# Kernel tuning notes

Hardware: AMD Instinct MI355X
Metric: run time of the kernel (lower is better)

## Reference

```python
import jax, jax.numpy as jnp
import numpy as np

D_MODEL = 2048
NUM_HEADS = 16
THETA = 10000.0


def setup_inputs() -> dict:
    key = jax.random.key(0)
    ks = jax.random.split(key, 5)
    bs, S, d = 4, 2048, D_MODEL
    std = (2.0 / (d + d)) ** 0.5
    x = jax.random.normal(ks[0], (bs, S, d), dtype=jnp.float32)
    wq = jax.random.normal(ks[1], (d, d), dtype=jnp.float32) * std
    wk = jax.random.normal(ks[2], (d, d), dtype=jnp.float32) * std
    wv = jax.random.normal(ks[3], (d, d), dtype=jnp.float32) * std
    wo = jax.random.normal(ks[4], (d, d), dtype=jnp.float32) * std
    return {"x": x, "wq": wq, "wk": wk, "wv": wv, "wo": wo}


def _rope(t, cos, sin):
    # t: (bs, H, S, d_k); cos/sin: (S, d_k) interleaved-duplicated
    # rotate_half: (-x1, x0, -x3, x2, ...)
    x_even = t[..., 0::2]
    x_odd = t[..., 1::2]
    rot = jnp.stack((-x_odd, x_even), axis=-1).reshape(t.shape)
    return t * cos + rot * sin


def reference(x, wq, wk, wv, wo):
    bs, S, d = x.shape
    H = NUM_HEADS
    dk = d // H
    # QKV projections (Linear has no bias; weight stored (out, in), applied as x @ W.T)
    q = (x @ wq.T).reshape(bs, S, H, dk).transpose(0, 2, 1, 3)  # (bs,H,S,dk)
    k = (x @ wk.T).reshape(bs, S, H, dk).transpose(0, 2, 1, 3)
    v = (x @ wv.T).reshape(bs, S, H, dk).transpose(0, 2, 1, 3)

    # RoPE tables (interleaved convention)
    half = dk // 2
    inv_freq = THETA ** (-2.0 * jnp.arange(half, dtype=jnp.float32) / dk)  # (half,)
    pos = jnp.arange(S, dtype=jnp.float32)
    ang = pos[:, None] * inv_freq[None, :]  # (S, half)
    cos = jnp.repeat(jnp.cos(ang), 2, axis=-1)  # (S, dk), (c0,c0,c1,c1,...)
    sin = jnp.repeat(jnp.sin(ang), 2, axis=-1)
    q = _rope(q, cos, sin)
    k = _rope(k, cos, sin)

    scale = 1.0 / jnp.sqrt(jnp.asarray(dk, dtype=x.dtype))
    attn = jnp.einsum("bhqd,bhkd->bhqk", q, k) * scale  # (bs,H,S,S)
    causal = jnp.tril(jnp.ones((S, S), dtype=bool))
    attn = jnp.where(causal, attn, -jnp.inf)
    probs = jax.nn.softmax(attn, axis=-1)
    out = jnp.einsum("bhqk,bhkd->bhqd", probs, v)  # (bs,H,S,dk)
    out = out.transpose(0, 2, 1, 3).reshape(bs, S, d)
    return out @ wo.T
```

## Files before the change

### kernel.cpp

```cpp
#include <hip/hip_runtime.h>
#include <hip/hip_bf16.h>
#include <cstdint>
#include <cstddef>

typedef unsigned short u16;
typedef unsigned int u32;
typedef __attribute__((ext_vector_type(8))) short short8;
typedef __attribute__((ext_vector_type(4))) short bfx4;
typedef __attribute__((ext_vector_type(4))) float f32x4;

#define D_MODEL 2048
#define SEQ     2048
#define BATCH   4
#define NHEADS  16
#define DKH     128
#define NTOK    (BATCH*SEQ)

typedef const __attribute__((address_space(1))) void* gptr_t;
typedef __attribute__((address_space(3))) void* lptr_t;

__device__ inline float bf2f(u16 u) {
  union { float f; u32 i; } x; x.i = ((u32)u) << 16; return x.f;
}
__device__ inline u16 f2bf(float f) {
  union { float f; u32 i; } x; x.f = f;
  return (u16)((x.i + 0x7FFFu + ((x.i >> 16) & 1u)) >> 16);
}
__device__ inline u32 packbf2(float a, float b) {
  union { float f; u32 i; } xa, xb; xa.f = a; xb.f = b;
  return (xa.i >> 16) | (xb.i & 0xFFFF0000u);
}

__global__ void cvt_kernel(const float* __restrict__ in, u16* __restrict__ out, int n8) {
  int i = blockIdx.x * 256 + threadIdx.x;
  if (i >= n8) return;
  const float* p = in + (size_t)i * 8;
  short8 v;
#pragma unroll
  for (int j = 0; j < 8; ++j) v[j] = (short)f2bf(p[j]);
  *(short8*)(out + (size_t)i * 8) = v;
}

__global__ void trig_kernel(float* __restrict__ cosT, float* __restrict__ sinT) {
  int i = blockIdx.x * 256 + threadIdx.x;
  int s = i >> 6, j = i & 63;
  float inv = powf(10000.0f, -2.0f * (float)j / 128.0f);
  float ang = (float)s * inv;
  cosT[i] = cosf(ang);
  sinT[i] = sinf(ang);
}

template<int F32OUT>
__global__ __launch_bounds__(512, 2)
void gemm_bt256(const u16* __restrict__ A, const u16* __restrict__ B,
                void* __restrict__ Cv, int M, int N, int K) {
  __shared__ u16 lds[2][2][256 * 64];
  const int T = threadIdx.x;
  const int lane = T & 63, w = T >> 6;
  const int lo = lane & 15, hi = lane >> 4;
  const int wr = w >> 2, wc = w & 3;
  const int id = blockIdx.x;
  const int bm = (id >> 3) * 256, bn = (id & 7) * 256;
  const int nt = K >> 6;

  const int qrow_base = (w & 3) * 8 + (w >> 2) * 128;
  const int lrow = lane >> 3;
  const int lchunk = lane & 7;

  auto STAGEQ = [&](int buf, int z, int kt) {
    int r0 = z * 32 + qrow_base;
    int rn = r0 + lrow;
    int ck = lchunk ^ (rn & 7);
    __builtin_amdgcn_global_load_lds(
        (gptr_t)(A + (size_t)(bm + rn) * K + kt * 64 + ck * 8),
        (lptr_t)(&lds[buf][0][0] + r0 * 64), 16, 0, 0);
    __builtin_amdgcn_global_load_lds(
        (gptr_t)(B + (size_t)(bn + rn) * K + kt * 64 + ck * 8),
        (lptr_t)(&lds[buf][1][0] + r0 * 64), 16, 0, 0);
  };

  f32x4 acc[8][4] = {};
  short8 bfrag[4][2];

#define GPHASE(qq, tt, cc) do {                                                \
    short8 af[2][2];                                                           \
    _Pragma("unroll")                                                          \
    for (int m2 = 0; m2 < 2; ++m2) {                                           \
      int row = wr * 128 + (2 * (qq) + m2) * 16 + lo;                          \
      _Pragma("unroll")                                                        \
      for (int c = 0; c < 2; ++c)                                              \
        af[m2][c] = *(const short8*)((const char*)&lds[cc][0][0] +             \
            (row << 7) + ((c * 64 + hi * 16) ^ ((row & 7) << 4)));             \
    }                                                                          \
    if ((qq) == 0) {                                                           \
      _Pragma("unroll")                                                        \
      for (int ni = 0; ni < 4; ++ni) {                                         \
        int row = wc * 64 + ni * 16 + lo;                                      \
        _Pragma("unroll")                                                      \
        for (int c = 0; c < 2; ++c)                                            \
          bfrag[ni][c] = *(const short8*)((const char*)&lds[cc][1][0] +        \
              (row << 7) + ((c * 64 + hi * 16) ^ ((row & 7) << 4)));           \
      }                                                                        \
    }                                                                          \
    { int zz = ((qq) + 3) & 3;                                                 \
      int stt = (qq) == 0 ? (tt) + 1 : (tt) + 2;                               \
      int sbuf = (qq) == 0 ? ((tt) + 1) & 1 : (tt) & 1;                        \
      if (stt < nt) STAGEQ(sbuf, zz, stt); }                                   \
    __builtin_amdgcn_s_barrier();                                              \
    asm volatile("s_waitcnt lgkmcnt(0)" ::: "memory");                         \
    __builtin_amdgcn_sched_barrier(0);                                         \
    __builtin_amdgcn_s_setprio(1);                                             \
    _Pragma("unroll")                                                          \
    for (int m2 = 0; m2 < 2; ++m2)                                             \
      _Pragma("unroll")                                                        \
      for (int ni = 0; ni < 4; ++ni)                                           \
        _Pragma("unroll")                                                      \
        for (int c = 0; c < 2; ++c)                                            \
          acc[2 * (qq) + m2][ni] = __builtin_amdgcn_mfma_f32_16x16x32_bf16(    \
              af[m2][c], bfrag[ni][c], acc[2 * (qq) + m2][ni], 0, 0, 0);       \
    __builtin_amdgcn_s_setprio(0);                                             \
    __builtin_amdgcn_sched_barrier(0);                                         \
    __builtin_amdgcn_s_barrier();                                              \
  } while (0)

#pragma unroll
  for (int z = 0; z < 4; ++z) STAGEQ(0, z, 0);
#pragma unroll
  for (int z = 0; z < 3; ++z) STAGEQ(1, z, 1);
  asm volatile("s_waitcnt vmcnt(6)" ::: "memory");
  __builtin_amdgcn_s_barrier();

  for (int t = 0; t < nt; ++t) {
    const int cur = t & 1;
    GPHASE(0, t, cur);
    GPHASE(1, t, cur);
    GPHASE(2, t, cur);
    GPHASE(3, t, cur);
    if (t == nt - 2) asm volatile("s_waitcnt vmcnt(0)" ::: "memory");
    else             asm volatile("s_waitcnt vmcnt(6)" ::: "memory");
    __builtin_amdgcn_s_barrier();
  }
#undef GPHASE

#pragma unroll
  for (int mi = 0; mi < 8; ++mi)
#pragma unroll
    for (int ni = 0; ni < 4; ++ni) {
      int row = bm + wr * 128 + mi * 16 + hi * 4;
      int col = bn + wc * 64 + ni * 16 + lo;
#pragma unroll
      for (int r = 0; r < 4; ++r) {
        if (F32OUT)
          ((float*)Cv)[(size_t)(row + r) * N + col] = acc[mi][ni][r];
        else
          ((u16*)Cv)[(size_t)(row + r) * N + col] = f2bf(acc[mi][ni][r]);
      }
    }
}

__global__ void rope_kernel(u16* __restrict__ t, const float* __restrict__ cosT,
                            const float* __restrict__ sinT, float premul) {
  int i = blockIdx.x * 256 + threadIdx.x;
  int row = i >> 8;
  int g = i & 255;
  int s = row & (SEQ - 1);
  int col = g << 3;
  int j0 = (col & 127) >> 1;
  short8 v = *(short8*)(t + (size_t)row * D_MODEL + col);
#pragma unroll
  for (int p = 0; p < 4; ++p) {
    float c  = cosT[s * 64 + j0 + p];
    float sn = sinT[s * 64 + j0 + p];
    float e = bf2f((u16)v[2 * p]), o = bf2f((u16)v[2 * p + 1]);
    v[2 * p]     = (short)f2bf((e * c - o * sn) * premul);
    v[2 * p + 1] = (short)f2bf((o * c + e * sn) * premul);
  }
  *(short8*)(t + (size_t)row * D_MODEL + col) = v;
}

__global__ void vt_kernel(const u16* __restrict__ V, u16* __restrict__ VT) {
  __shared__ u16 tbuf[64][66];
  int bh = blockIdx.z;
  int b = bh >> 4, h = bh & 15;
  int s0 = blockIdx.x << 6, d0 = blockIdx.y << 6;
  for (int i = threadIdx.x; i < 512; i += 256) {
    int sr = i >> 3, c8 = (i & 7) << 3;
    short8 v = *(const short8*)(V + (size_t)(b * SEQ + s0 + sr) * D_MODEL + h * DKH + d0 + c8);
#pragma unroll
    for (int j = 0; j < 8; ++j) tbuf[sr][c8 + j] = (u16)v[j];
  }
  __syncthreads();
  for (int i = threadIdx.x; i < 512; i += 256) {
    int dr = i >> 3, s8 = (i & 7) << 3;
    short8 v;
#pragma unroll
    for (int j = 0; j < 8; ++j) v[j] = (short)tbuf[s8 + j][dr];
    *(short8*)(VT + ((size_t)bh * DKH + d0 + dr) * SEQ + s0 + s8) = v;
  }
}

__device__ __forceinline__ void attn_qtile(
    int qt, int b, int h, int bh,
    const u16* __restrict__ Q, const u16* __restrict__ K,
    const u16* __restrict__ VT, u16* __restrict__ O,
    u16 (*Ksb)[64 * 128], u16 (*Vsb)[128 * 64], u16* Pw)
{
  const int T = threadIdx.x, lane = T & 63, w = T >> 6;
  const int lo = lane & 15, hi = lane >> 4;
  const int q0 = qt << 6;
  const int qrow = q0 + w * 16 + lo;
  const int swzC = (lo & 7) << 4;

  const u16* Qp = Q + (size_t)(b * SEQ + qrow) * D_MODEL + h * DKH;
  short8 qf[4];
#pragma unroll
  for (int c = 0; c < 4; ++c) qf[c] = *(const short8*)(Qp + c * 32 + hi * 8);

  f32x4 ot[8] = {};
  float m = -1e30f, l = 0.f;

  const u16* Kbase = K + ((size_t)b * SEQ) * D_MODEL + h * DKH;
  const u16* Vbase = VT + (size_t)bh * DKH * SEQ;

  auto STAGE = [&](int buf, int kt2) {
    const int kb2 = kt2 << 6;
#pragma unroll
    for (int q = 0; q < 4; ++q) {
      int base = q * 256 + (T & 192);
      int s = base + lane;
      int kv = s >> 4, ck = (s & 15) ^ (kv & 7);
      __builtin_amdgcn_global_load_lds(
          (gptr_t)(Kbase + (size_t)(kb2 + kv) * D_MODEL + ck * 8),
          (lptr_t)(Ksb[buf] + (size_t)base * 8), 16, 0, 0);
      int d = s >> 3, cv2 = (s & 7) ^ (d & 7);
      __builtin_amdgcn_global_load_lds(
          (gptr_t)(Vbase + (size_t)d * SEQ + kb2 + cv2 * 8),
          (lptr_t)(Vsb[buf] + (size_t)base * 8), 16, 0, 0);
    }
  };

  STAGE(0, 0);
  __syncthreads();
  int cur = 0;

  for (int kt = 0; kt <= qt; ++kt) {
    if (kt < qt) STAGE(cur ^ 1, kt + 1);
    const int kb = kt << 6;
    const u16* Ks = Ksb[cur];
    const u16* Vs = Vsb[cur];

    f32x4 sa[4];
    __builtin_amdgcn_s_setprio(1);
#pragma unroll
    for (int g = 0; g < 4; ++g) {
      f32x4 s4 = {0.f, 0.f, 0.f, 0.f};
      int krow = g * 16 + lo;
#pragma unroll
      for (int c = 0; c < 4; ++c) {
        int o = ((krow << 8) + c * 64 + hi * 16) ^ ((krow & 7) << 4);
        short8 kf = *(const short8*)((const char*)Ks + o);
        s4 = __builtin_amdgcn_mfma_f32_16x16x32_bf16(kf, qf[c], s4, 0, 0, 0);
      }
      sa[g] = s4;
    }
    __builtin_amdgcn_s_setprio(0);

    const bool diag = (kt == qt);
    float pm = -1e30f;
#pragma unroll
    for (int g = 0; g < 4; ++g)
#pragma unroll
      for (int r = 0; r < 4; ++r) {
        float sv = sa[g][r];
        if (diag && (kb + g * 16 + hi * 4 + r) > qrow) sv = -1e30f;
        sa[g][r] = sv;
        pm = fmaxf(pm, sv);
      }
    pm = fmaxf(pm, __shfl_xor(pm, 16));
    pm = fmaxf(pm, __shfl_xor(pm, 32));

    if (!__all(pm <= m + 8.0f)) {
      float mn = fmaxf(m, pm);
      float sc = __builtin_amdgcn_exp2f(m - mn);
      l *= sc;
#pragma unroll
      for (int g2 = 0; g2 < 8; ++g2)
#pragma unroll
        for (int r = 0; r < 4; ++r) ot[g2][r] *= sc;
      m = mn;
    }

    float rs = 0.f;
#pragma unroll
    for (int g = 0; g < 4; ++g) {
      float p0 = __builtin_amdgcn_exp2f(sa[g][0] - m);
      float p1 = __builtin_amdgcn_exp2f(sa[g][1] - m);
      float p2 = __builtin_amdgcn_exp2f(sa[g][2] - m);
      float p3 = __builtin_amdgcn_exp2f(sa[g][3] - m);
      rs += (p0 + p1) + (p2 + p3);
      int off = lo * 128 + ((g * 32 + hi * 8) ^ swzC);
      *(u32*)((char*)Pw + off)     = packbf2(p0, p1);
      *(u32*)((char*)Pw + off + 4) = packbf2(p2, p3);
    }
    rs += __shfl_xor(rs, 16);
    rs += __shfl_xor(rs, 32);
    l += rs;

    __builtin_amdgcn_s_setprio(1);
#pragma unroll
    for (int c2 = 0; c2 < 2; ++c2) {
      short8 pf = *(const short8*)((char*)Pw + lo * 128 + ((c2 * 64 + hi * 16) ^ swzC));
#pragma unroll
      for (int g2 = 0; g2 < 8; ++g2) {
        int vrow = g2 * 16 + lo;
        int vo = ((vrow << 7) + c2 * 64 + hi * 16) ^ ((vrow & 7) << 4);
        short8 vf = *(const short8*)((const char*)Vs + vo);
        ot[g2] = __builtin_amdgcn_mfma_f32_16x16x32_bf16(vf, pf, ot[g2], 0, 0, 0);
      }
    }
    __builtin_amdgcn_s_setprio(0);

    __syncthreads();
    cur ^= 1;
  }

  float invl = 1.0f / l;
  u16* Op = O + (size_t)(b * SEQ + qrow) * D_MODEL + h * DKH + hi * 4;
#pragma unroll
  for (int g2 = 0; g2 < 8; ++g2) {
    bfx4 v4;
#pragma unroll
    for (int r = 0; r < 4; ++r) v4[r] = (short)f2bf(ot[g2][r] * invl);
    *(bfx4*)(Op + g2 * 16) = v4;
  }
}

__global__ __launch_bounds__(256)
void attn_kernel(const u16* __restrict__ Q, const u16* __restrict__ K,
                 const u16* __restrict__ VT, u16* __restrict__ O) {
  __shared__ u16 Ksb[2][64 * 128];
  __shared__ u16 Vsb[2][128 * 64];
  __shared__ u16 Ps[4 * 16 * 64];
  const int wg = blockIdx.x;
  const int xcd = wg & 7, idx = wg >> 3;
  const int bh = xcd * 8 + (idx >> 4);
  const int pair = idx & 15;
  const int b = bh >> 4, h = bh & 15;
  u16* Pw = Ps + (threadIdx.x >> 6) * 1024;
#pragma unroll 1
  for (int side = 0; side < 2; ++side) {
    const int qt = side ? pair : 31 - pair;
    attn_qtile(qt, b, h, bh, Q, K, VT, O, Ksb, Vsb, Pw);
  }
}

extern "C" void kernel_launch(void* const* d_in, const int* in_sizes, int n_in,
                              void* d_out, int out_size, void* d_ws, size_t ws_size,
                              hipStream_t stream) {
  const float* x  = (const float*)d_in[0];
  const float* wq = (const float*)d_in[1];
  const float* wk = (const float*)d_in[2];
  const float* wv = (const float*)d_in[3];
  const float* wo = (const float*)d_in[4];
  float* out = (float*)d_out;

  const size_t TOKB = (size_t)NTOK * D_MODEL * 2;
  const size_t WB   = (size_t)D_MODEL * D_MODEL * 2;
  char* p = (char*)d_ws;
  u16* xb  = (u16*)p; p += TOKB;
  u16* wqb = (u16*)p; p += WB;
  u16* wkb = (u16*)p; p += WB;
  u16* wvb = (u16*)p; p += WB;
  u16* wob = (u16*)p; p += WB;
  u16* Qb  = (u16*)p; p += TOKB;
  u16* Kb  = (u16*)p; p += TOKB;
  u16* Vb  = (u16*)p; p += TOKB;
  u16* VTb = (u16*)p; p += TOKB;
  u16* Ob  = (u16*)p; p += TOKB;
  float* cosT = (float*)p; p += (size_t)SEQ * 64 * 4;
  float* sinT = (float*)p; p += (size_t)SEQ * 64 * 4;

  cvt_kernel<<<8192, 256, 0, stream>>>(x,  xb,  2097152);
  cvt_kernel<<<2048, 256, 0, stream>>>(wq, wqb, 524288);
  cvt_kernel<<<2048, 256, 0, stream>>>(wk, wkb, 524288);
  cvt_kernel<<<2048, 256, 0, stream>>>(wv, wvb, 524288);
  cvt_kernel<<<2048, 256, 0, stream>>>(wo, wob, 524288);
  trig_kernel<<<512, 256, 0, stream>>>(cosT, sinT);

  gemm_bt256<0><<<256, 512, 0, stream>>>(xb, wqb, Qb, NTOK, D_MODEL, D_MODEL);
  gemm_bt256<0><<<256, 512, 0, stream>>>(xb, wkb, Kb, NTOK, D_MODEL, D_MODEL);
  gemm_bt256<0><<<256, 512, 0, stream>>>(xb, wvb, Vb, NTOK, D_MODEL, D_MODEL);

  rope_kernel<<<8192, 256, 0, stream>>>(Qb, cosT, sinT,
      0.08838834764831845f * 1.4426950408889634f);
  rope_kernel<<<8192, 256, 0, stream>>>(Kb, cosT, sinT, 1.0f);

  vt_kernel<<<dim3(32, 2, 64), 256, 0, stream>>>(Vb, VTb);

  attn_kernel<<<1024, 256, 0, stream>>>(Qb, Kb, VTb, Ob);

  gemm_bt256<1><<<256, 512, 0, stream>>>(Ob, wob, out, NTOK, D_MODEL, D_MODEL);
}
```

Baseline: 488.2 us.

## Single-buffer attention K/V with split staging, fuse Q RoPE, batch weight conversion

The attention kernel now uses single K and V LDS buffers. K and V loads are issued separately: the next K tile loads during the softmax phase and the next V tile after the PV MFMAs, with explicit vmcnt waits and barriers. Halving LDS use allows four blocks per CU, per the new launch bounds. Q RoPE and scaling move into the attention Q-fragment load, dropping one rope pass, and the four weight conversions merge into one launch. The risk is less latency hiding per block, which depends on the extra occupancy and the finer-grained syncs to compensate.

```diff
diff --git a/kernel.cpp b/kernel.cpp
--- a/kernel.cpp
+++ b/kernel.cpp
@@ -19,6 +19,11 @@
 typedef const __attribute__((address_space(1))) void* gptr_t;
 typedef __attribute__((address_space(3))) void* lptr_t;
 
+#define SBAR() do { __builtin_amdgcn_sched_barrier(0); \
+                    __builtin_amdgcn_s_barrier();      \
+                    __builtin_amdgcn_sched_barrier(0); } while (0)
+#define VMCNT(n) asm volatile("s_waitcnt vmcnt(" #n ")" ::: "memory")
+
 __device__ inline float bf2f(u16 u) {
   union { float f; u32 i; } x; x.i = ((u32)u) << 16; return x.f;
 }
@@ -39,6 +44,19 @@
 #pragma unroll
   for (int j = 0; j < 8; ++j) v[j] = (short)f2bf(p[j]);
   *(short8*)(out + (size_t)i * 8) = v;
+}
+
+__global__ void cvtw_kernel(const float* __restrict__ wq, const float* __restrict__ wk,
+                            const float* __restrict__ wv, const float* __restrict__ wo,
+                            u16* __restrict__ wall) {
+  int by = blockIdx.y;
+  const float* src = by == 0 ? wq : by == 1 ? wk : by == 2 ? wv : wo;
+  int i = blockIdx.x * 256 + threadIdx.x;
+  const float* p = src + (size_t)i * 8;
+  short8 v;
+#pragma unroll
+  for (int j = 0; j < 8; ++j) v[j] = (short)f2bf(p[j]);
+  *(short8*)(wall + (size_t)by * D_MODEL * D_MODEL + (size_t)i * 8) = v;
 }
 
 __global__ void trig_kernel(float* __restrict__ cosT, float* __restrict__ sinT) {
@@ -203,18 +221,33 @@
     int qt, int b, int h, int bh,
     const u16* __restrict__ Q, const u16* __restrict__ K,
     const u16* __restrict__ VT, u16* __restrict__ O,
-    u16 (*Ksb)[64 * 128], u16 (*Vsb)[128 * 64], u16* Pw)
+    const float* __restrict__ cosT, const float* __restrict__ sinT,
+    u16* Ks, u16* Vs, u16* Pw)
 {
   const int T = threadIdx.x, lane = T & 63, w = T >> 6;
   const int lo = lane & 15, hi = lane >> 4;
   const int q0 = qt << 6;
   const int qrow = q0 + w * 16 + lo;
   const int swzC = (lo & 7) << 4;
+  const float SC = 0.08838834764831845f * 1.4426950408889634f;
 
   const u16* Qp = Q + (size_t)(b * SEQ + qrow) * D_MODEL + h * DKH;
+  const float* cp = cosT + qrow * 64;
+  const float* sp = sinT + qrow * 64;
   short8 qf[4];
 #pragma unroll
-  for (int c = 0; c < 4; ++c) qf[c] = *(const short8*)(Qp + c * 32 + hi * 8);
+  for (int c = 0; c < 4; ++c) {
+    short8 v = *(const short8*)(Qp + c * 32 + hi * 8);
+#pragma unroll
+    for (int p = 0; p < 4; ++p) {
+      float cc = cp[c * 16 + hi * 4 + p] * SC;
+      float sn = sp[c * 16 + hi * 4 + p] * SC;
+      float e = bf2f((u16)v[2 * p]), o = bf2f((u16)v[2 * p + 1]);
+      v[2 * p]     = (short)f2bf(e * cc - o * sn);
+      v[2 * p + 1] = (short)f2bf(o * cc + e * sn);
+    }
+    qf[c] = v;
+  }
 
   f32x4 ot[8] = {};
   float m = -1e30f, l = 0.f;
@@ -222,7 +255,7 @@
   const u16* Kbase = K + ((size_t)b * SEQ) * D_MODEL + h * DKH;
   const u16* Vbase = VT + (size_t)bh * DKH * SEQ;
 
-  auto STAGE = [&](int buf, int kt2) {
+  auto STAGE_K = [&](int kt2) {
     const int kb2 = kt2 << 6;
 #pragma unroll
     for (int q = 0; q < 4; ++q) {
@@ -231,23 +264,31 @@
       int kv = s >> 4, ck = (s & 15) ^ (kv & 7);
       __builtin_amdgcn_global_load_lds(
           (gptr_t)(Kbase + (size_t)(kb2 + kv) * D_MODEL + ck * 8),
-          (lptr_t)(Ksb[buf] + (size_t)base * 8), 16, 0, 0);
+          (lptr_t)(Ks + (size_t)base * 8), 16, 0, 0);
+    }
+  };
+  auto STAGE_V = [&](int kt2) {
+    const int kb2 = kt2 << 6;
+#pragma unroll
+    for (int q = 0; q < 4; ++q) {
+      int base = q * 256 + (T & 192);
+      int s = base + lane;
       int d = s >> 3, cv2 = (s & 7) ^ (d & 7);
       __builtin_amdgcn_global_load_lds(
           (gptr_t)(Vbase + (size_t)d * SEQ + kb2 + cv2 * 8),
-          (lptr_t)(Vsb[buf] + (size_t)base * 8), 16, 0, 0);
+          (lptr_t)(Vs + (size_t)base * 8), 16, 0, 0);
     }
   };
 
-  STAGE(0, 0);
-  __syncthreads();
-  int cur = 0;
+  SBAR();
+  STAGE_K(0);
+  STAGE_V(0);
+  VMCNT(0);
+  SBAR();
 
   for (int kt = 0; kt <= qt; ++kt) {
-    if (kt < qt) STAGE(cur ^ 1, kt + 1);
     const int kb = kt << 6;
-    const u16* Ks = Ksb[cur];
-    const u16* Vs = Vsb[cur];
+    if (kt > 0) { VMCNT(4); SBAR(); }
 
     f32x4 sa[4];
     __builtin_amdgcn_s_setprio(1);
@@ -264,6 +305,9 @@
       sa[g] = s4;
     }
     __builtin_amdgcn_s_setprio(0);
+
+    SBAR();
+    if (kt < qt) STAGE_K(kt + 1);
 
     const bool diag = (kt == qt);
     float pm = -1e30f;
@@ -306,6 +350,11 @@
     rs += __shfl_xor(rs, 32);
     l += rs;
 
+    if (kt > 0) {
+      if (kt < qt) { VMCNT(4); } else { VMCNT(0); }
+      SBAR();
+    }
+
     __builtin_amdgcn_s_setprio(1);
 #pragma unroll
     for (int c2 = 0; c2 < 2; ++c2) {
@@ -320,8 +369,10 @@
     }
     __builtin_amdgcn_s_setprio(0);
 
-    __syncthreads();
-    cur ^= 1;
+    if (kt < qt) {
+      SBAR();
+      STAGE_V(kt + 1);
+    }
   }
 
   float invl = 1.0f / l;
@@ -335,11 +386,12 @@
   }
 }
 
-__global__ __launch_bounds__(256)
+__global__ __launch_bounds__(256, 4)
 void attn_kernel(const u16* __restrict__ Q, const u16* __restrict__ K,
-                 const u16* __restrict__ VT, u16* __restrict__ O) {
-  __shared__ u16 Ksb[2][64 * 128];
-  __shared__ u16 Vsb[2][128 * 64];
+                 const u16* __restrict__ VT, u16* __restrict__ O,
+                 const float* __restrict__ cosT, const float* __restrict__ sinT) {
+  __shared__ u16 Ks[64 * 128];
+  __shared__ u16 Vs[128 * 64];
   __shared__ u16 Ps[4 * 16 * 64];
   const int wg = blockIdx.x;
   const int xcd = wg & 7, idx = wg >> 3;
@@ -350,7 +402,7 @@
 #pragma unroll 1
   for (int side = 0; side < 2; ++side) {
     const int qt = side ? pair : 31 - pair;
-    attn_qtile(qt, b, h, bh, Q, K, VT, O, Ksb, Vsb, Pw);
+    attn_qtile(qt, b, h, bh, Q, K, VT, O, cosT, sinT, Ks, Vs, Pw);
   }
 }
 
@@ -380,24 +432,19 @@
   float* cosT = (float*)p; p += (size_t)SEQ * 64 * 4;
   float* sinT = (float*)p; p += (size_t)SEQ * 64 * 4;
 
-  cvt_kernel<<<8192, 256, 0, stream>>>(x,  xb,  2097152);
-  cvt_kernel<<<2048, 256, 0, stream>>>(wq, wqb, 524288);
-  cvt_kernel<<<2048, 256, 0, stream>>>(wk, wkb, 524288);
-  cvt_kernel<<<2048, 256, 0, stream>>>(wv, wvb, 524288);
-  cvt_kernel<<<2048, 256, 0, stream>>>(wo, wob, 524288);
+  cvt_kernel<<<8192, 256, 0, stream>>>(x, xb, 2097152);
+  cvtw_kernel<<<dim3(2048, 4), 256, 0, stream>>>(wq, wk, wv, wo, wqb);
   trig_kernel<<<512, 256, 0, stream>>>(cosT, sinT);
 
   gemm_bt256<0><<<256, 512, 0, stream>>>(xb, wqb, Qb, NTOK, D_MODEL, D_MODEL);
   gemm_bt256<0><<<256, 512, 0, stream>>>(xb, wkb, Kb, NTOK, D_MODEL, D_MODEL);
   gemm_bt256<0><<<256, 512, 0, stream>>>(xb, wvb, Vb, NTOK, D_MODEL, D_MODEL);
 
-  rope_kernel<<<8192, 256, 0, stream>>>(Qb, cosT, sinT,
-      0.08838834764831845f * 1.4426950408889634f);
   rope_kernel<<<8192, 256, 0, stream>>>(Kb, cosT, sinT, 1.0f);
 
   vt_kernel<<<dim3(32, 2, 64), 256, 0, stream>>>(Vb, VTb);
 
-  attn_kernel<<<1024, 256, 0, stream>>>(Qb, Kb, VTb, Ob);
+  attn_kernel<<<1024, 256, 0, stream>>>(Qb, Kb, VTb, Ob, cosT, sinT);
 
   gemm_bt256<1><<<256, 512, 0, stream>>>(Ob, wob, out, NTOK, D_MODEL, D_MODEL);
 }
```

Result: slower. 517.9 us (+6.1%).
